# Kernel optimization log

Hardware: AMD Instinct MI355X
Metric: run time of the kernel (lower is better)

The kernel has to match this reference:

```python
import jax, jax.numpy as jnp
from jax import lax
import numpy as np

HID = 100
SEQ = 480
INP = 640
NCLS = 307200  # 480*640
NLAYERS = 4
NSTAGES = 3


def setup_inputs() -> dict:
    key = jax.random.key(0)
    ks = jax.random.split(key, 12)
    s = 0.05
    return {
        "x":    jax.random.normal(ks[0], (1, SEQ, INP), jnp.float32),
        "xn":   jax.random.normal(ks[1], (1, SEQ, INP), jnp.float32),
        "xnn":  jax.random.normal(ks[2], (1, SEQ, INP), jnp.float32),
        # layer-0 input weights per stage: (stage, 4H, input)
        "Wih0": jax.random.normal(ks[3], (NSTAGES, 4 * HID, INP), jnp.float32) * s,
        # layers 1..3 input weights: (stage, 3, 4H, H)
        "WihR": jax.random.normal(ks[4], (NSTAGES, NLAYERS - 1, 4 * HID, HID), jnp.float32) * s,
        # recurrent weights: (stage, 4, 4H, H)
        "Whh":  jax.random.normal(ks[5], (NSTAGES, NLAYERS, 4 * HID, HID), jnp.float32) * s,
        "bih":  jax.random.normal(ks[6], (NSTAGES, NLAYERS, 4 * HID), jnp.float32) * s,
        "bhh":  jax.random.normal(ks[7], (NSTAGES, NLAYERS, 4 * HID), jnp.float32) * s,
        "fcW":  jax.random.normal(ks[8], (NSTAGES, NCLS, HID), jnp.float32) * s,
        "fcb":  jax.random.normal(ks[9], (NSTAGES, NCLS), jnp.float32) * s,
    }


def _lstm_layer(xseq, Wih, Whh, b):
    """One LSTM layer (PyTorch gate order i,f,g,o). xseq: (B,T,I) -> (B,T,H)."""
    # Precompute input projections for all timesteps (one big GEMM).
    xp = jnp.einsum('bti,gi->btg', xseq, Wih) + b  # (B,T,4H)
    B = xseq.shape[0]
    h0 = jnp.zeros((B, HID), xseq.dtype)
    c0 = jnp.zeros((B, HID), xseq.dtype)

    def step(carry, xt):
        h, c = carry
        g = xt + h @ Whh.T  # (B,4H)
        i, f, gg, o = jnp.split(g, 4, axis=-1)
        c = jax.nn.sigmoid(f) * c + jax.nn.sigmoid(i) * jnp.tanh(gg)
        h = jax.nn.sigmoid(o) * jnp.tanh(c)
        return (h, c), h

    _, hs = lax.scan(step, (h0, c0), jnp.swapaxes(xp, 0, 1))  # hs: (T,B,H)
    return jnp.swapaxes(hs, 0, 1)


def _forward(x, xn, xnn, Wih0, WihR, Whh, bih, bhh, fcW, fcb):
    blends = [xn, xnn, None]
    cur = x.reshape(-1, SEQ, INP)
    for s in range(NSTAGES):
        seq = cur
        for l in range(NLAYERS):
            Wih = Wih0[s] if l == 0 else WihR[s, l - 1]
            seq = _lstm_layer(seq, Wih, Whh[s, l], bih[s, l] + bhh[s, l])
        dec = seq[:, -1, :] @ fcW[s].T + fcb[s]  # (1, NCLS)
        cur = dec.reshape(1, SEQ, INP)
        if blends[s] is not None:
            cur = (cur + blends[s]) * 0.5
    return cur


def reference(x, xn, xnn, Wih0, WihR, Whh, bih, bhh, fcW, fcb):
    return _forward(x, xn, xnn, Wih0, WihR, Whh, bih, bhh, fcW, fcb)
```

## Files before the change

### kernel.cpp

```cpp
#include <hip/hip_runtime.h>
#include <hip/hip_bf16.h>

#define HID   100
#define SEQ   480
#define INP   640
#define NCLS  307200
#define G4    400
#define TILE  16
#define NTILE 30
#define RING  4

typedef float    v2    __attribute__((ext_vector_type(2)));
typedef _Float16 f16x8 __attribute__((ext_vector_type(8)));
typedef float    f32x4 __attribute__((ext_vector_type(4)));

__device__ __forceinline__ v2 fma2(v2 a, v2 b, v2 c) {
    return __builtin_elementwise_fma(a, b, c);
}
__device__ __forceinline__ float fast_sigmoid(float x) {
    return __builtin_amdgcn_rcpf(1.f + __expf(-x));
}
__device__ __forceinline__ float fast_tanh(float x) {
    return 1.f - 2.f * __builtin_amdgcn_rcpf(__expf(2.f * x) + 1.f);
}
__device__ __forceinline__ int ld_acq(const int* p) {
    return __hip_atomic_load(p, __ATOMIC_ACQUIRE, __HIP_MEMORY_SCOPE_AGENT);
}
__device__ __forceinline__ void st_rel(int* p, int v) {
    __hip_atomic_store(p, v, __ATOMIC_RELEASE, __HIP_MEMORY_SCOPE_AGENT);
}
__device__ __forceinline__ f16x8 zero8() {
    f16x8 v;
    #pragma unroll
    for (int i = 0; i < 8; ++i) v[i] = (_Float16)0.f;
    return v;
}
__device__ __forceinline__ f16x8 cvt8(float4 a, float4 b) {
    f16x8 v;
    v[0] = (_Float16)a.x; v[1] = (_Float16)a.y;
    v[2] = (_Float16)a.z; v[3] = (_Float16)a.w;
    v[4] = (_Float16)b.x; v[5] = (_Float16)b.y;
    v[6] = (_Float16)b.z; v[7] = (_Float16)b.w;
    return v;
}
__device__ __forceinline__ f16x8 cvt4z(float4 a) {
    f16x8 v = zero8();
    v[0] = (_Float16)a.x; v[1] = (_Float16)a.y;
    v[2] = (_Float16)a.z; v[3] = (_Float16)a.w;
    return v;
}

__global__ __launch_bounds__(256, 1) void stage_kernel(
    const float* __restrict__ xin,
    const float* __restrict__ Wih0,
    const float* __restrict__ WihR,
    const float* __restrict__ Whh,
    const float* __restrict__ bih,
    const float* __restrict__ bhh,
    float* __restrict__ ring,
    _Float16* __restrict__ hseq16,
    int* __restrict__ flags)
{
    const int bid = blockIdx.x;
    const int tid = threadIdx.x;
    int* hflag  = flags;
    int* rdflag = flags + 4;
    int* xpflag = flags + 8;

    if (bid >= 4) {
        const int p  = bid - 4;
        const int l  = p / NTILE;
        const int t  = p % NTILE;
        const int t0 = t * TILE;
        const int lane = tid & 63;
        const int wid  = tid >> 6;
        const int col  = lane & 15;
        const int kb   = lane >> 4;

        if (l > 0) { while (ld_acq(&hflag[l - 1]) < t0 + TILE) {} }
        if (t >= RING) { while (ld_acq(&rdflag[l]) < t - (RING - 1)) {} }

        float* slot = ring + ((size_t)l * RING + (t & (RING - 1))) * (TILE * G4);

        if (l == 0) {
            f16x8 af[20];
            const float* arow = xin + (size_t)(t0 + col) * INP;
            #pragma unroll
            for (int ks = 0; ks < 20; ++ks) {
                const float* ap = arow + ks * 32 + kb * 8;
                af[ks] = cvt8(*(const float4*)ap, *(const float4*)(ap + 4));
            }
            for (int tile = wid; tile < 25; tile += 4) {
                const int n = tile * 16 + col;
                const float* brow = Wih0 + (size_t)n * INP;
                const float bn = bih[n] + bhh[n];
                f32x4 acc = {bn, bn, bn, bn};
                #pragma unroll
                for (int ks = 0; ks < 20; ++ks) {
                    const float* bp = brow + ks * 32 + kb * 8;
                    f16x8 bf = cvt8(*(const float4*)bp, *(const float4*)(bp + 4));
                    acc = __builtin_amdgcn_mfma_f32_16x16x32_f16(af[ks], bf, acc, 0, 0, 0);
                }
                const int u = n % 100, g = n / 100;
                #pragma unroll
                for (int r = 0; r < 4; ++r)
                    slot[(size_t)(kb * 4 + r) * G4 + u * 4 + g] = acc[r];
            }
        } else {
            f16x8 af[4];
            const _Float16* arow = hseq16 + ((size_t)(l - 1) * SEQ + t0 + col) * 104;
            af[0] = *(const f16x8*)(arow + kb * 8);
            af[1] = *(const f16x8*)(arow + 32 + kb * 8);
            af[2] = *(const f16x8*)(arow + 64 + kb * 8);
            af[3] = (kb == 0) ? *(const f16x8*)(arow + 96) : zero8();
            for (int tile = wid; tile < 25; tile += 4) {
                const int n = tile * 16 + col;
                const float* brow = WihR + ((size_t)(l - 1) * G4 + n) * HID;
                const float bn = bih[l * G4 + n] + bhh[l * G4 + n];
                f32x4 acc = {bn, bn, bn, bn};
                #pragma unroll
                for (int ks = 0; ks < 3; ++ks) {
                    const float* bp = brow + ks * 32 + kb * 8;
                    f16x8 bf = cvt8(*(const float4*)bp, *(const float4*)(bp + 4));
                    acc = __builtin_amdgcn_mfma_f32_16x16x32_f16(af[ks], bf, acc, 0, 0, 0);
                }
                f16x8 bf3 = (kb == 0) ? cvt4z(*(const float4*)(brow + 96)) : zero8();
                acc = __builtin_amdgcn_mfma_f32_16x16x32_f16(af[3], bf3, acc, 0, 0, 0);
                const int u = n % 100, g = n / 100;
                #pragma unroll
                for (int r = 0; r < 4; ++r)
                    slot[(size_t)(kb * 4 + r) * G4 + u * 4 + g] = acc[r];
            }
        }
        __syncthreads();
        if (tid == 0) st_rel(&xpflag[p], 1);
        return;
    }

    __shared__ __align__(16) float xp_lds[TILE * G4];
    __shared__ __align__(16) float h_lds[128];
    __shared__ __align__(16) float4 parts[128];
    __shared__ __align__(16) _Float16 hist16[TILE * 104];

    const int l  = bid;
    const int kh = tid >> 7;
    const int j  = tid & 127;
    const int k0 = kh * 52;
    const bool own = (kh == 0) && (j < 100);

    v2 w2[4][26];
    #pragma unroll
    for (int g = 0; g < 4; ++g)
        #pragma unroll
        for (int cc = 0; cc < 26; ++cc) w2[g][cc] = v2{0.f, 0.f};
    if (j < 100) {
        const int nf4 = kh ? 12 : 13;
        #pragma unroll
        for (int g = 0; g < 4; ++g) {
            const float* row = Whh + ((size_t)(l * G4 + g * 100 + j)) * HID + k0;
            #pragma unroll
            for (int cc = 0; cc < 13; ++cc) {
                if (cc < nf4) {
                    float4 t4 = *(const float4*)(row + 4 * cc);
                    w2[g][2 * cc]     = v2{t4.x, t4.y};
                    w2[g][2 * cc + 1] = v2{t4.z, t4.w};
                }
            }
        }
    }
    if (tid < 128) h_lds[tid] = 0.f;
    for (int i = tid; i < TILE * 104; i += 256) hist16[i] = (_Float16)0.f;
    float c = 0.f;
    __syncthreads();

    for (int t = 0; t < NTILE; ++t) {
        while (ld_acq(&xpflag[l * NTILE + t]) < 1) {}
        {
            const float4* src = (const float4*)(ring +
                ((size_t)l * RING + (t & (RING - 1))) * (TILE * G4));
            float4* dst = (float4*)xp_lds;
            for (int i = tid; i < TILE * G4 / 4; i += 256) dst[i] = src[i];
        }
        __syncthreads();
        if (tid == 0) st_rel(&rdflag[l], t + 1);

        for (int tt = 0; tt < TILE; ++tt) {
            float4 hs[13];
            const float4* hp = (const float4*)(h_lds + k0);
            #pragma unroll
            for (int cc = 0; cc < 13; ++cc) hs[cc] = hp[cc];

            v2 a0 = {0.f, 0.f}, a1 = {0.f, 0.f};
            v2 a2 = {0.f, 0.f}, a3 = {0.f, 0.f};
            #pragma unroll
            for (int cc = 0; cc < 13; ++cc) {
                v2 lo = v2{hs[cc].x, hs[cc].y};
                v2 hi = v2{hs[cc].z, hs[cc].w};
                a0 = fma2(w2[0][2 * cc], lo, a0);
                a1 = fma2(w2[1][2 * cc], lo, a1);
                a2 = fma2(w2[2][2 * cc], lo, a2);
                a3 = fma2(w2[3][2 * cc], lo, a3);
                a0 = fma2(w2[0][2 * cc + 1], hi, a0);
                a1 = fma2(w2[1][2 * cc + 1], hi, a1);
                a2 = fma2(w2[2][2 * cc + 1], hi, a2);
                a3 = fma2(w2[3][2 * cc + 1], hi, a3);
            }
            if (kh == 1 && j < 100)
                parts[j] = make_float4(a0[0] + a0[1], a1[0] + a1[1],
                                       a2[0] + a2[1], a3[0] + a3[1]);
            __syncthreads();

            if (own) {
                float4 q  = parts[j];
                float4 xq = *(const float4*)(xp_lds + tt * G4 + (j << 2));
                float gi = a0[0] + a0[1] + q.x + xq.x;
                float gf = a1[0] + a1[1] + q.y + xq.y;
                float gg = a2[0] + a2[1] + q.z + xq.z;
                float go = a3[0] + a3[1] + q.w + xq.w;
                float si = fast_sigmoid(gi);
                float sf = fast_sigmoid(gf);
                float so = fast_sigmoid(go);
                float tg = fast_tanh(gg);
                c = sf * c + si * tg;
                float h = so * fast_tanh(c);
                h_lds[j] = h;
                hist16[tt * 104 + j] = (_Float16)h;
            }
            __syncthreads();
        }

        {
            const uint* hsrc = (const uint*)hist16;
            uint* hdst = (uint*)(hseq16 + ((size_t)l * SEQ + t * TILE) * 104);
            for (int i = tid; i < TILE * 52; i += 256) hdst[i] = hsrc[i];
        }
        __syncthreads();
        if (tid == 0) st_rel(&hflag[l], (t + 1) * TILE);
    }
}

__global__ __launch_bounds__(256) void fc_blend(
    const _Float16* __restrict__ hlast,
    const float* __restrict__ fcW,
    const float* __restrict__ fcb,
    const float* __restrict__ blend,
    float* __restrict__ outp, int do_blend)
{
    __shared__ __align__(16) float h_lds[HID + 4];
    const int tid = threadIdx.x;
    if (tid < 104) h_lds[tid] = (tid < 100) ? (float)hlast[tid] : 0.f;
    __syncthreads();

    const int cidx = blockIdx.x * 256 + tid;
    const float4* wr = reinterpret_cast<const float4*>(fcW + (size_t)cidx * HID);
    float acc = fcb[cidx];
    #pragma unroll
    for (int k = 0; k < 25; ++k) {
        float4 w4 = wr[k];
        float4 h4 = reinterpret_cast<const float4*>(h_lds)[k];
        acc = fmaf(w4.x, h4.x, acc);
        acc = fmaf(w4.y, h4.y, acc);
        acc = fmaf(w4.z, h4.z, acc);
        acc = fmaf(w4.w, h4.w, acc);
    }
    if (do_blend) acc = (acc + blend[cidx]) * 0.5f;
    outp[cidx] = acc;
}

extern "C" void kernel_launch(void* const* d_in, const int* in_sizes, int n_in,
                              void* d_out, int out_size, void* d_ws, size_t ws_size,
                              hipStream_t stream)
{
    const float* x    = (const float*)d_in[0];
    const float* xn   = (const float*)d_in[1];
    const float* xnn  = (const float*)d_in[2];
    const float* Wih0 = (const float*)d_in[3];
    const float* WihR = (const float*)d_in[4];
    const float* Whh  = (const float*)d_in[5];
    const float* bih  = (const float*)d_in[6];
    const float* bhh  = (const float*)d_in[7];
    const float* fcW  = (const float*)d_in[8];
    const float* fcb  = (const float*)d_in[9];
    float* outp = (float*)d_out;
    float* ws = (float*)d_ws;

    float*     ring   = ws;
    _Float16*  hseq16 = (_Float16*)(ws + 102400);
    float*     cur    = ws + 102400 + 99840;
    int*       flags  = (int*)(ws + 102400 + 99840 + 307200);

    hipMemsetAsync(flags, 0, 3 * 128 * sizeof(int), stream);

    for (int s = 0; s < 3; ++s) {
        const float* stage_in = (s == 0) ? x : cur;

        stage_kernel<<<4 + 4 * NTILE, 256, 0, stream>>>(
            stage_in,
            Wih0 + (size_t)s * G4 * INP,
            WihR + (size_t)s * 3 * G4 * HID,
            Whh  + (size_t)s * 4 * G4 * HID,
            bih  + (size_t)s * 4 * G4,
            bhh  + (size_t)s * 4 * G4,
            ring, hseq16, flags + s * 128);

        const float* blend = (s == 0) ? xn : (s == 1) ? xnn : nullptr;
        float* dst = (s == 2) ? outp : cur;
        fc_blend<<<NCLS / 256, 256, 0, stream>>>(
            hseq16 + ((size_t)3 * SEQ + SEQ - 1) * 104,
            fcW + (size_t)s * NCLS * HID, fcb + (size_t)s * NCLS,
            blend, dst, (s < 2) ? 1 : 0);
    }
}
```

Before: 1.916 ms.

## Split input-projection blocks in half, broadcast h via readlane, add polling sleeps

The input-projection producer blocks are split into two halves per time tile, giving 240 producer blocks that each handle half the gate columns and signal completion with an atomic counter. Consumers now wait for a count of two. The recurrent step no longer loads 13 float4s of h from LDS per thread. Each lane loads one float4 and the others get it through readlane broadcasts, and h history is kept per timestep in a 17-row LDS buffer that replaces the separate fp16 history. Spin loops gain s_sleep to cut memory polling pressure. The changes target latency on the serial recurrence and the producer critical path, at the cost of more blocks, scalar readlane traffic, and a possible wake-up delay from the sleeps.

```diff
diff --git a/kernel.cpp b/kernel.cpp
--- a/kernel.cpp
+++ b/kernel.cpp
@@ -29,6 +29,9 @@
 __device__ __forceinline__ void st_rel(int* p, int v) {
     __hip_atomic_store(p, v, __ATOMIC_RELEASE, __HIP_MEMORY_SCOPE_AGENT);
 }
+__device__ __forceinline__ float rdlane(float v, int l) {
+    return __uint_as_float(__builtin_amdgcn_readlane(__float_as_uint(v), l));
+}
 __device__ __forceinline__ f16x8 zero8() {
     f16x8 v;
     #pragma unroll
@@ -49,6 +52,9 @@
     v[2] = (_Float16)a.z; v[3] = (_Float16)a.w;
     return v;
 }
+
+#define HVAL(hv, DD) rdlane(((DD & 3) == 0 ? (hv).x : (DD & 3) == 1 ? (hv).y \
+                             : (DD & 3) == 2 ? (hv).z : (hv).w), (DD) >> 2)
 
 __global__ __launch_bounds__(256, 1) void stage_kernel(
     const float* __restrict__ xin,
@@ -69,16 +75,24 @@
 
     if (bid >= 4) {
         const int p  = bid - 4;
-        const int l  = p / NTILE;
-        const int t  = p % NTILE;
+        const int l  = p / 60;
+        const int r6 = p % 60;
+        const int t  = r6 >> 1;
+        const int nh = r6 & 1;
         const int t0 = t * TILE;
         const int lane = tid & 63;
         const int wid  = tid >> 6;
         const int col  = lane & 15;
         const int kb   = lane >> 4;
-
-        if (l > 0) { while (ld_acq(&hflag[l - 1]) < t0 + TILE) {} }
-        if (t >= RING) { while (ld_acq(&rdflag[l]) < t - (RING - 1)) {} }
+        const int tile_lo = nh * 13;
+        const int tile_hi = nh ? 25 : 13;
+
+        if (l > 0) {
+            while (ld_acq(&hflag[l - 1]) < t0 + TILE) __builtin_amdgcn_s_sleep(8);
+        }
+        if (t >= RING) {
+            while (ld_acq(&rdflag[l]) < t - (RING - 1)) __builtin_amdgcn_s_sleep(8);
+        }
 
         float* slot = ring + ((size_t)l * RING + (t & (RING - 1))) * (TILE * G4);
 
@@ -90,7 +104,7 @@
                 const float* ap = arow + ks * 32 + kb * 8;
                 af[ks] = cvt8(*(const float4*)ap, *(const float4*)(ap + 4));
             }
-            for (int tile = wid; tile < 25; tile += 4) {
+            for (int tile = tile_lo + wid; tile < tile_hi; tile += 4) {
                 const int n = tile * 16 + col;
                 const float* brow = Wih0 + (size_t)n * INP;
                 const float bn = bih[n] + bhh[n];
@@ -113,7 +127,7 @@
             af[1] = *(const f16x8*)(arow + 32 + kb * 8);
             af[2] = *(const f16x8*)(arow + 64 + kb * 8);
             af[3] = (kb == 0) ? *(const f16x8*)(arow + 96) : zero8();
-            for (int tile = wid; tile < 25; tile += 4) {
+            for (int tile = tile_lo + wid; tile < tile_hi; tile += 4) {
                 const int n = tile * 16 + col;
                 const float* brow = WihR + ((size_t)(l - 1) * G4 + n) * HID;
                 const float bn = bih[l * G4 + n] + bhh[l * G4 + n];
@@ -133,19 +147,21 @@
             }
         }
         __syncthreads();
-        if (tid == 0) st_rel(&xpflag[p], 1);
+        if (tid == 0)
+            __hip_atomic_fetch_add(&xpflag[l * NTILE + t], 1, __ATOMIC_RELEASE,
+                                   __HIP_MEMORY_SCOPE_AGENT);
         return;
     }
 
     __shared__ __align__(16) float xp_lds[TILE * G4];
-    __shared__ __align__(16) float h_lds[128];
-    __shared__ __align__(16) float4 parts[128];
-    __shared__ __align__(16) _Float16 hist16[TILE * 104];
-
-    const int l  = bid;
-    const int kh = tid >> 7;
-    const int j  = tid & 127;
-    const int k0 = kh * 52;
+    __shared__ __align__(16) float h_lds[17 * 128];
+    __shared__ __align__(16) float4 parts[104];
+
+    const int l    = bid;
+    const int kh   = tid >> 7;
+    const int j    = tid & 127;
+    const int lane = tid & 63;
+    const int k0   = kh * 52;
     const bool own = (kh == 0) && (j < 100);
 
     v2 w2[4][26];
@@ -168,13 +184,21 @@
             }
         }
     }
-    if (tid < 128) h_lds[tid] = 0.f;
-    for (int i = tid; i < TILE * 104; i += 256) hist16[i] = (_Float16)0.f;
+    #pragma unroll
+    for (int g = 0; g < 4; ++g)
+        #pragma unroll
+        for (int cc = 0; cc < 26; ++cc)
+            asm volatile("" : "+v"(w2[g][cc]));
+
+    for (int i = tid; i < 17 * 128; i += 256) h_lds[i] = 0.f;
     float c = 0.f;
+    _Float16* hseq_own = hseq16 + (size_t)l * SEQ * 104;
     __syncthreads();
 
     for (int t = 0; t < NTILE; ++t) {
-        while (ld_acq(&xpflag[l * NTILE + t]) < 1) {}
+        const int t0 = t * TILE;
+
+        while (ld_acq(&xpflag[l * NTILE + t]) < 2) __builtin_amdgcn_s_sleep(8);
         {
             const float4* src = (const float4*)(ring +
                 ((size_t)l * RING + (t & (RING - 1))) * (TILE * G4));
@@ -185,25 +209,19 @@
         if (tid == 0) st_rel(&rdflag[l], t + 1);
 
         for (int tt = 0; tt < TILE; ++tt) {
-            float4 hs[13];
-            const float4* hp = (const float4*)(h_lds + k0);
-            #pragma unroll
-            for (int cc = 0; cc < 13; ++cc) hs[cc] = hp[cc];
+            float4 hv = *(const float4*)(h_lds + tt * 128 + k0 + ((lane & 15) << 2));
+            float4 xq = own ? *(const float4*)(xp_lds + tt * G4 + (j << 2))
+                            : make_float4(0.f, 0.f, 0.f, 0.f);
 
             v2 a0 = {0.f, 0.f}, a1 = {0.f, 0.f};
             v2 a2 = {0.f, 0.f}, a3 = {0.f, 0.f};
             #pragma unroll
-            for (int cc = 0; cc < 13; ++cc) {
-                v2 lo = v2{hs[cc].x, hs[cc].y};
-                v2 hi = v2{hs[cc].z, hs[cc].w};
-                a0 = fma2(w2[0][2 * cc], lo, a0);
-                a1 = fma2(w2[1][2 * cc], lo, a1);
-                a2 = fma2(w2[2][2 * cc], lo, a2);
-                a3 = fma2(w2[3][2 * cc], lo, a3);
-                a0 = fma2(w2[0][2 * cc + 1], hi, a0);
-                a1 = fma2(w2[1][2 * cc + 1], hi, a1);
-                a2 = fma2(w2[2][2 * cc + 1], hi, a2);
-                a3 = fma2(w2[3][2 * cc + 1], hi, a3);
+            for (int pp = 0; pp < 26; ++pp) {
+                v2 hh = v2{HVAL(hv, 2 * pp), HVAL(hv, 2 * pp + 1)};
+                a0 = fma2(w2[0][pp], hh, a0);
+                a1 = fma2(w2[1][pp], hh, a1);
+                a2 = fma2(w2[2][pp], hh, a2);
+                a3 = fma2(w2[3][pp], hh, a3);
             }
             if (kh == 1 && j < 100)
                 parts[j] = make_float4(a0[0] + a0[1], a1[0] + a1[1],
@@ -211,8 +229,7 @@
             __syncthreads();
 
             if (own) {
-                float4 q  = parts[j];
-                float4 xq = *(const float4*)(xp_lds + tt * G4 + (j << 2));
+                float4 q = parts[j];
                 float gi = a0[0] + a0[1] + q.x + xq.x;
                 float gf = a1[0] + a1[1] + q.y + xq.y;
                 float gg = a2[0] + a2[1] + q.z + xq.z;
@@ -223,19 +240,21 @@
                 float tg = fast_tanh(gg);
                 c = sf * c + si * tg;
                 float h = so * fast_tanh(c);
-                h_lds[j] = h;
-                hist16[tt * 104 + j] = (_Float16)h;
+                h_lds[(tt + 1) * 128 + j] = h;
             }
             __syncthreads();
         }
 
-        {
-            const uint* hsrc = (const uint*)hist16;
-            uint* hdst = (uint*)(hseq16 + ((size_t)l * SEQ + t * TILE) * 104);
-            for (int i = tid; i < TILE * 52; i += 256) hdst[i] = hsrc[i];
-        }
+        for (int i = tid; i < 2048; i += 256) {
+            const int rr = i >> 7, uu = i & 127;
+            if (uu < 104) {
+                float hval = (uu < 100) ? h_lds[(rr + 1) * 128 + uu] : 0.f;
+                hseq_own[(size_t)(t0 + rr) * 104 + uu] = (_Float16)hval;
+            }
+        }
+        if (tid < 128) h_lds[tid] = h_lds[16 * 128 + tid];
         __syncthreads();
-        if (tid == 0) st_rel(&hflag[l], (t + 1) * TILE);
+        if (tid == 0) st_rel(&hflag[l], t0 + TILE);
     }
 }
 
@@ -294,7 +313,7 @@
     for (int s = 0; s < 3; ++s) {
         const float* stage_in = (s == 0) ? x : cur;
 
-        stage_kernel<<<4 + 4 * NTILE, 256, 0, stream>>>(
+        stage_kernel<<<4 + 240, 256, 0, stream>>>(
             stage_in,
             Wih0 + (size_t)s * G4 * INP,
             WihR + (size_t)s * 3 * G4 * HID,
```

New measurement: 3.276 ms. +71.0%, slower.
